# Kernel optimization log

Measured on AMD Instinct MI355X. Metric: run time of the kernel, lower is better.

## Reference

```python
import jax, jax.numpy as jnp
import numpy as np

B, D_IN, H, NZ, NC = 32768, 768, 2048, 128, 1024
EPS, NITERS = 0.5, 15


def setup_inputs() -> dict:
    key = jax.random.key(0)
    ks = jax.random.split(key, 4)
    x = jax.random.normal(ks[0], (B, D_IN), jnp.float32)
    # scaled init so feature magnitudes keep exp(-dist/eps) in f32 range
    W1 = jax.random.normal(ks[1], (D_IN, H), jnp.float32) / np.sqrt(D_IN)
    b1 = jnp.zeros((H,), jnp.float32)
    W2 = jax.random.normal(ks[2], (H, NZ), jnp.float32) / np.sqrt(H)
    b2 = jnp.zeros((NZ,), jnp.float32)
    centroids = jax.random.normal(ks[3], (NC, NZ), jnp.float32)
    return {
        'x': x, 'W1': W1, 'b1': b1, 'W2': W2, 'b2': b2,
        'centroids': centroids,
        'cluster_counts': jnp.zeros((NC,), jnp.int32),
        'raw_counts': jnp.zeros((NC,), jnp.int32),
        'total_soft_counts': jnp.zeros((NC,), jnp.float32),
    }


def _sinkhorn(scores, eps=EPS, niters=NITERS):
    # scores: [B, K].  Q: [K, B], matches torch reference where sum(Q) = col-sums.
    Q = jnp.exp(scores / eps).T
    Q = Q / jnp.sum(Q, axis=0, keepdims=True)
    K, Bb = Q.shape
    r = 1.0 / K
    c = 1.0 / Bb

    def body(Q, _):
        Q = Q * (r / jnp.sum(Q, axis=1))[:, None]
        Q = Q * (c / jnp.sum(Q, axis=0))[None, :]
        return Q, None

    Q, _ = jax.lax.scan(body, Q, None, length=niters)
    return (Q / jnp.sum(Q, axis=0, keepdims=True)).T  # [B, K]


def reference(x, W1, b1, W2, b2, centroids, cluster_counts, raw_counts, total_soft_counts):
    # fc backbone: Linear -> ReLU -> Linear
    fv = jax.nn.relu(x @ W1 + b1) @ W2 + b2                        # [B, nz]
    # pairwise euclidean distances to centroids (cdist via gram trick;
    # avoids materializing the [B, nc, nz] broadcast torch creates)
    sq = (jnp.sum(fv * fv, axis=1)[:, None]
          + jnp.sum(centroids * centroids, axis=1)[None, :]
          - 2.0 * fv @ centroids.T)
    cluster_dists = jnp.sqrt(jnp.maximum(sq, 1e-12))               # [B, nc]

    # sinkhorn branch (no_grad in torch)
    soft_assignments = jax.lax.stop_gradient(_sinkhorn(-cluster_dists))
    batch_assignments = jnp.argmin(soft_assignments, axis=1)       # [B]
    soft_counts = jnp.sum(soft_assignments, axis=0)                # [nc]
    # soft_train=False: gather assigned distances
    loss = jnp.mean(jnp.take_along_axis(cluster_dists, batch_assignments[:, None], axis=1))

    # scatter-accumulate counts
    new_raw = raw_counts.at[jnp.argmin(cluster_dists, axis=1)].add(1)
    new_cluster = cluster_counts.at[batch_assignments].add(1)
    new_total_soft = total_soft_counts + soft_counts
    return loss, batch_assignments, soft_counts, new_raw, new_cluster, new_total_soft
```

## Files before the change

### kernel.cpp

```cpp
#include <hip/hip_runtime.h>
#include <math.h>

#define BN    32768
#define DIN   768
#define HN    2048
#define NZ    128
#define NCN   1024

typedef __attribute__((ext_vector_type(8))) short s16x8;
typedef __attribute__((ext_vector_type(4))) float f32x4;
typedef unsigned short u16;

#define MFMA16(a,b,c) __builtin_amdgcn_mfma_f32_16x16x32_bf16(a,b,c,0,0,0)

__device__ __forceinline__ u16 bf16_rne(float x){
  unsigned u = __float_as_uint(x);
  unsigned r = (u + 0x7FFFu + ((u >> 16) & 1u)) >> 16;
  return (u16)r;
}
__device__ __forceinline__ float bf16_tof(u16 h){
  return __uint_as_float(((unsigned)h) << 16);
}
__device__ __forceinline__ void split3(float x, u16& h, u16& m, u16& l){
  h = bf16_rne(x);
  float r1 = x - bf16_tof(h);
  m = bf16_rne(r1);
  float r2 = r1 - bf16_tof(m);
  l = bf16_rne(r2);
}

__device__ __forceinline__ void gload16(const void* gsrc, void* lds){
  __builtin_amdgcn_global_load_lds(
      (const __attribute__((address_space(1))) unsigned int*)gsrc,
      (__attribute__((address_space(3))) unsigned int*)lds, 16, 0, 0);
}

__global__ __launch_bounds__(1024) void k0_init(float* u, int* hraw, int* hclu){
  const int k = threadIdx.x;
  u[k] = 1.0f;
  hraw[k] = 0;
  hclu[k] = 0;
}

__global__ __launch_bounds__(256) void c_split(
    const float* __restrict__ in, u16* __restrict__ oh, u16* __restrict__ om,
    u16* __restrict__ ol, int n4)
{
  const int i = blockIdx.x*256 + threadIdx.x;
  if (i >= n4) return;
  const f32x4 v = *(const f32x4*)&in[(size_t)i*4];
  ushort4 h4, m4, l4;
  split3(v[0], h4.x, m4.x, l4.x);
  split3(v[1], h4.y, m4.y, l4.y);
  split3(v[2], h4.z, m4.z, l4.z);
  split3(v[3], h4.w, m4.w, l4.w);
  *(ushort4*)&oh[(size_t)i*4] = h4;
  *(ushort4*)&om[(size_t)i*4] = m4;
  *(ushort4*)&ol[(size_t)i*4] = l4;
}

__global__ __launch_bounds__(256) void c_tsplit(
    const float* __restrict__ in, int R, int C,
    u16* __restrict__ oh, u16* __restrict__ om, u16* __restrict__ ol)
{
  __shared__ float L[64][65];
  const int t = threadIdx.x;
  const int bi = blockIdx.x, bj = blockIdx.y;
  #pragma unroll
  for (int m=0;m<4;++m){
    int flat = t + 256*m;
    int r = flat >> 4, c4 = (flat & 15) << 2;
    const float4 v = *(const float4*)&in[(size_t)(bi*64 + r)*C + bj*64 + c4];
    L[r][c4+0] = v.x; L[r][c4+1] = v.y; L[r][c4+2] = v.z; L[r][c4+3] = v.w;
  }
  __syncthreads();
  #pragma unroll
  for (int m=0;m<4;++m){
    int flat = t + 256*m;
    int oc = flat >> 4, k4 = (flat & 15) << 2;
    ushort4 h4, m4, l4;
    split3(L[k4+0][oc], h4.x, m4.x, l4.x);
    split3(L[k4+1][oc], h4.y, m4.y, l4.y);
    split3(L[k4+2][oc], h4.z, m4.z, l4.z);
    split3(L[k4+3][oc], h4.w, m4.w, l4.w);
    size_t off = (size_t)(bj*64 + oc)*R + bi*64 + k4;
    *(ushort4*)&oh[off] = h4;
    *(ushort4*)&om[off] = m4;
    *(ushort4*)&ol[off] = l4;
  }
}

__global__ __launch_bounds__(256) void c_norm(
    const float* __restrict__ in, float* __restrict__ out)
{
  const int w = threadIdx.x >> 6, l = threadIdx.x & 63;
  const int row = blockIdx.x*4 + w;
  const float2 v = *(const float2*)&in[(size_t)row*128 + l*2];
  float s = v.x*v.x + v.y*v.y;
  #pragma unroll
  for (int off=32; off; off>>=1) s += __shfl_xor(s, off, 64);
  if (l == 0) out[row] = s;
}

__global__ __launch_bounds__(256, 2) void k1_mfma(
    const u16* __restrict__ Xh, const u16* __restrict__ Xm, const u16* __restrict__ Xl,
    const u16* __restrict__ W1h, const u16* __restrict__ W1m, const u16* __restrict__ W1l,
    const float* __restrict__ b1,
    const u16* __restrict__ W2h, const u16* __restrict__ W2m, const u16* __restrict__ W2l,
    const float* __restrict__ b2, float* __restrict__ fv)
{
  __shared__ __align__(16) unsigned char sm[73728];
  unsigned char* xsr = sm;
  unsigned char* wsr = sm + 24576;

  const int t  = threadIdx.x;
  const int l  = t & 63;
  const int wn = t >> 6;
  const int g  = (l >> 4) & 3;
  const int lr = l & 15;
  const int row0 = blockIdx.x * 64;

  f32x4 fvacc[4][2];
  #pragma unroll
  for (int mf=0;mf<4;++mf){
    fvacc[mf][0] = (f32x4){0.f,0.f,0.f,0.f};
    fvacc[mf][1] = (f32x4){0.f,0.f,0.f,0.f};
  }

  #pragma unroll 1
  for (int nc = 0; nc < 16; ++nc){
    f32x4 a1acc[4][2];
    #pragma unroll
    for (int mf=0;mf<4;++mf){
      a1acc[mf][0] = (f32x4){0.f,0.f,0.f,0.f};
      a1acc[mf][1] = (f32x4){0.f,0.f,0.f,0.f};
    }

    #pragma unroll 1
    for (int ks = 0; ks < 12; ++ks){
      #pragma unroll
      for (int i=0;i<6;++i){
        const int ci = wn*6 + i;
        const int s  = ci >> 3;
        const int rb = ci & 7;
        const int xr = rb*8 + (l >> 3);
        const int q  = l & 7;
        const u16* Xp = (s==0) ? Xh : ((s==1) ? Xm : Xl);
        const u16* src = Xp + (size_t)(row0 + xr)*768 + ks*64 + ((q ^ (xr & 7)) << 3);
        gload16(src, xsr + s*8192 + rb*1024);
      }
      #pragma unroll
      for (int i=0;i<12;++i){
        const int ci = wn*12 + i;
        const int s  = ci >> 4;
        const int rb = ci & 15;
        const int rloc = rb*8 + (l >> 3);
        const int q  = l & 7;
        const u16* Wp = (s==0) ? W1h : ((s==1) ? W1m : W1l);
        const u16* src = Wp + (size_t)(nc*128 + rloc)*768 + ks*64 + ((q ^ (rloc & 7)) << 3);
        gload16(src, wsr + s*16384 + rb*1024);
      }
      __syncthreads();

      #pragma unroll
      for (int kk=0;kk<2;++kk){
        s16x8 Bf[3][2], Af[3][4];
        #pragma unroll
        for (int s=0;s<3;++s){
          #pragma unroll
          for (int nf=0;nf<2;++nf){
            const int br = wn*32 + nf*16 + lr;
            Bf[s][nf] = *(const s16x8*)(wsr + s*16384 + br*128 + ((16*(g + 4*kk)) ^ ((br & 7) << 4)));
          }
          #pragma unroll
          for (int mf=0;mf<4;++mf){
            const int ar = mf*16 + lr;
            Af[s][mf] = *(const s16x8*)(xsr + s*8192 + ar*128 + ((16*(g + 4*kk)) ^ ((ar & 7) << 4)));
          }
        }
        #pragma unroll
        for (int mf=0;mf<4;++mf){
          #pragma unroll
          for (int nf=0;nf<2;++nf){
            f32x4 acc = a1acc[mf][nf];
            acc = MFMA16(Af[0][mf], Bf[0][nf], acc);
            acc = MFMA16(Af[0][mf], Bf[1][nf], acc);
            acc = MFMA16(Af[1][mf], Bf[0][nf], acc);
            acc = MFMA16(Af[1][mf], Bf[1][nf], acc);
            acc = MFMA16(Af[0][mf], Bf[2][nf], acc);
            acc = MFMA16(Af[2][mf], Bf[0][nf], acc);
            a1acc[mf][nf] = acc;
          }
        }
      }
      __syncthreads();
    }

    const float b1v0 = b1[nc*128 + wn*32 + lr];
    const float b1v1 = b1[nc*128 + wn*32 + 16 + lr];

    #pragma unroll
    for (int half=0; half<2; ++half){
      if ((wn >> 1) == half){
        #pragma unroll
        for (int mf=0;mf<4;++mf){
          #pragma unroll
          for (int nf=0;nf<2;++nf){
            const int klocal = (wn & 1)*32 + nf*16 + lr;
            #pragma unroll
            for (int r=0;r<4;++r){
              float vv = a1acc[mf][nf][r] + ((nf==0) ? b1v0 : b1v1);
              vv = vv > 0.f ? vv : 0.f;
              u16 sh, sm2, sl;
              split3(vv, sh, sm2, sl);
              const int ar = mf*16 + g*4 + r;
              const int bo = ar*128 + ((2*klocal) ^ ((ar & 7) << 4));
              *(u16*)(xsr + bo)         = sh;
              *(u16*)(xsr + 8192 + bo)  = sm2;
              *(u16*)(xsr + 16384 + bo) = sl;
            }
          }
        }
      }
      #pragma unroll
      for (int i=0;i<12;++i){
        const int ci = wn*12 + i;
        const int s  = ci >> 4;
        const int rb = ci & 15;
        const int rloc = rb*8 + (l >> 3);
        const int q  = l & 7;
        const u16* Wp = (s==0) ? W2h : ((s==1) ? W2m : W2l);
        const u16* src = Wp + (size_t)rloc*2048 + nc*128 + half*64 + ((q ^ (rloc & 7)) << 3);
        gload16(src, wsr + s*16384 + rb*1024);
      }
      __syncthreads();

      #pragma unroll
      for (int kk=0;kk<2;++kk){
        s16x8 Bf[3][2], Af[3][4];
        #pragma unroll
        for (int s=0;s<3;++s){
          #pragma unroll
          for (int nf=0;nf<2;++nf){
            const int br = wn*32 + nf*16 + lr;
            Bf[s][nf] = *(const s16x8*)(wsr + s*16384 + br*128 + ((16*(g + 4*kk)) ^ ((br & 7) << 4)));
          }
          #pragma unroll
          for (int mf=0;mf<4;++mf){
            const int ar = mf*16 + lr;
            Af[s][mf] = *(const s16x8*)(xsr + s*8192 + ar*128 + ((16*(g + 4*kk)) ^ ((ar & 7) << 4)));
          }
        }
        #pragma unroll
        for (int mf=0;mf<4;++mf){
          #pragma unroll
          for (int nf=0;nf<2;++nf){
            f32x4 acc = fvacc[mf][nf];
            acc = MFMA16(Af[0][mf], Bf[0][nf], acc);
            acc = MFMA16(Af[0][mf], Bf[1][nf], acc);
            acc = MFMA16(Af[1][mf], Bf[0][nf], acc);
            acc = MFMA16(Af[1][mf], Bf[1][nf], acc);
            acc = MFMA16(Af[0][mf], Bf[2][nf], acc);
            acc = MFMA16(Af[2][mf], Bf[0][nf], acc);
            fvacc[mf][nf] = acc;
          }
        }
      }
      __syncthreads();
    }
  }

  const float b2v0 = b2[wn*32 + lr];
  const float b2v1 = b2[wn*32 + 16 + lr];
  #pragma unroll
  for (int mf=0;mf<4;++mf){
    #pragma unroll
    for (int nf=0;nf<2;++nf){
      #pragma unroll
      for (int r=0;r<4;++r){
        const int frow = row0 + mf*16 + g*4 + r;
        const int col  = wn*32 + nf*16 + lr;
        fv[(size_t)frow*NZ + col] = fvacc[mf][nf][r] + ((nf==0) ? b2v0 : b2v1);
      }
    }
  }
}

__global__ __launch_bounds__(256, 2) void k2_mfma(
    const u16* __restrict__ fvh, const u16* __restrict__ fvm, const u16* __restrict__ fvl,
    const u16* __restrict__ ch,  const u16* __restrict__ cm,  const u16* __restrict__ cl,
    const float* __restrict__ fvn, const float* __restrict__ cn,
    float* __restrict__ Q0)
{
  __shared__ __align__(16) unsigned char bs[49152];
  __shared__ float cnl[NCN];
  const int t  = threadIdx.x;
  const int l  = t & 63;
  const int wn = t >> 6;
  const int g  = (l >> 4) & 3;
  const int lr = l & 15;
  const int row0 = blockIdx.x * 64;
  const int arow = row0 + wn*16 + lr;

  s16x8 Af[3][4];
  #pragma unroll
  for (int kk=0;kk<4;++kk){
    const size_t ao = (size_t)arow*128 + kk*32 + g*8;
    Af[0][kk] = *(const s16x8*)&fvh[ao];
    Af[1][kk] = *(const s16x8*)&fvm[ao];
    Af[2][kk] = *(const s16x8*)&fvl[ao];
  }
  #pragma unroll
  for (int m=0;m<4;++m) cnl[t + 256*m] = cn[t + 256*m];
  const f32x4 fvnv = *(const f32x4*)&fvn[row0 + wn*16 + g*4];

  #pragma unroll 1
  for (int cc = 0; cc < NCN; cc += 64){
    #pragma unroll
    for (int i=0;i<12;++i){
      const int ci = wn*12 + i;
      const int s  = ci >> 4;
      const int rb = ci & 15;
      const int crow = rb*4 + (l >> 4);
      const int q  = l & 15;
      const u16* Cp = (s==0) ? ch : ((s==1) ? cm : cl);
      const u16* src = Cp + (size_t)(cc + crow)*128 + ((q ^ (crow & 15)) << 3);
      gload16(src, bs + s*16384 + rb*1024);
    }
    __syncthreads();

    f32x4 acc[4];
    #pragma unroll
    for (int nf=0;nf<4;++nf) acc[nf] = (f32x4){0.f,0.f,0.f,0.f};

    #pragma unroll
    for (int kk=0;kk<4;++kk){
      s16x8 Bq[3][4];
      #pragma unroll
      for (int nf=0;nf<4;++nf){
        const int br = nf*16 + lr;
        const int base = br*256 + (((g + 4*kk) ^ (br & 15)) << 4);
        Bq[0][nf] = *(const s16x8*)(bs + base);
        Bq[1][nf] = *(const s16x8*)(bs + 16384 + base);
        Bq[2][nf] = *(const s16x8*)(bs + 32768 + base);
      }
      #pragma unroll
      for (int nf=0;nf<4;++nf){
        f32x4 a = acc[nf];
        a = MFMA16(Af[0][kk], Bq[0][nf], a);
        a = MFMA16(Af[0][kk], Bq[1][nf], a);
        a = MFMA16(Af[1][kk], Bq[0][nf], a);
        a = MFMA16(Af[1][kk], Bq[1][nf], a);
        a = MFMA16(Af[0][kk], Bq[2][nf], a);
        a = MFMA16(Af[2][kk], Bq[0][nf], a);
        acc[nf] = a;
      }
    }

    #pragma unroll
    for (int nf=0;nf<4;++nf){
      const int n = cc + nf*16 + lr;
      const float cv = cnl[n];
      #pragma unroll
      for (int r=0;r<4;++r){
        float sq = fvnv[r] + cv - 2.0f*acc[nf][r];
        sq = sq > 1e-12f ? sq : 1e-12f;
        const float d = sqrtf(sq);
        Q0[(size_t)(row0 + wn*16 + g*4 + r)*NCN + n] = expf(-2.0f*d);
      }
    }
    __syncthreads();
  }
}

__global__ __launch_bounds__(256) void k3_pass(
    const float* __restrict__ Q0, const float* __restrict__ u,
    float* __restrict__ S_part, float alpha)
{
  __shared__ __align__(16) float ul[NCN];
  __shared__ __align__(16) float Sw[4][NCN];
  const int t = threadIdx.x;
  const int w = t >> 6, l = t & 63;
  #pragma unroll
  for (int m=0;m<4;++m) ul[t + 256*m] = u[t + 256*m];
  #pragma unroll
  for (int m=0;m<16;++m) (&Sw[0][0])[t + 256*m] = 0.f;
  __syncthreads();

  const float4* ul4 = (const float4*)ul;
  float4* Sw4 = (float4*)&Sw[w][0];
  const int gw = blockIdx.x*4 + w;
  const size_t b0 = (size_t)gw * 16;
  for (int rr=0; rr<16; ++rr){
    const float4* qrow = (const float4*)(Q0 + (b0 + rr)*NCN);
    float4 q4[4];
    float part = 0.f;
    #pragma unroll
    for (int j=0;j<4;++j){
      q4[j] = qrow[l + 64*j];
      float4 uu = ul4[l + 64*j];
      part += q4[j].x*uu.x; part += q4[j].y*uu.y;
      part += q4[j].z*uu.z; part += q4[j].w*uu.w;
    }
    #pragma unroll
    for (int off=32; off; off>>=1) part += __shfl_xor(part, off, 64);
    const float v = alpha / part;
    #pragma unroll
    for (int j=0;j<4;++j){
      float4 s = Sw4[l + 64*j];
      s.x += q4[j].x*v; s.y += q4[j].y*v; s.z += q4[j].z*v; s.w += q4[j].w*v;
      Sw4[l + 64*j] = s;
    }
  }
  __syncthreads();
  #pragma unroll
  for (int m=0;m<4;++m){
    int k = t + 256*m;
    S_part[(size_t)blockIdx.x*NCN + k] = ((Sw[0][k]+Sw[1][k])+(Sw[2][k]+Sw[3][k]));
  }
}

__global__ __launch_bounds__(256) void k4_unew(
    const float* __restrict__ S_part, float* __restrict__ u)
{
  __shared__ float P[4][64];
  const int t = threadIdx.x;
  const int col = blockIdx.x*64 + (t & 63);
  const int s4 = t >> 6;
  float p = 0.f;
  for (int i=0;i<128;++i)
    p += S_part[(size_t)(s4*128 + i)*NCN + col];
  P[s4][t & 63] = p;
  __syncthreads();
  if (s4 == 0){
    float tot = ((P[0][t] + P[1][t]) + (P[2][t] + P[3][t]));
    u[col] = (1.0f/1024.0f) / tot;
  }
}

__device__ __forceinline__ float comp4(const float4 v, int c){
  return (c==0)?v.x:(c==1)?v.y:(c==2)?v.z:v.w;
}

__global__ __launch_bounds__(256) void k5_final(
    const float* __restrict__ Q0, const float* __restrict__ u,
    float* __restrict__ softc_part, float* __restrict__ loss_part,
    int* __restrict__ hist_raw, int* __restrict__ hist_clu,
    float* __restrict__ out_ba)
{
  __shared__ __align__(16) float ul[NCN];
  __shared__ __align__(16) float Sw[4][NCN];
  __shared__ float lossw[4];
  const int t = threadIdx.x;
  const int w = t >> 6, l = t & 63;
  #pragma unroll
  for (int m=0;m<4;++m) ul[t + 256*m] = u[t + 256*m];
  #pragma unroll
  for (int m=0;m<16;++m) (&Sw[0][0])[t + 256*m] = 0.f;
  __syncthreads();

  const float4* ul4 = (const float4*)ul;
  float4* Sw4 = (float4*)&Sw[w][0];
  const int gw = blockIdx.x*4 + w;
  const size_t b0 = (size_t)gw * 32;
  float lacc = 0.f;
  for (int rr=0; rr<32; ++rr){
    const size_t b = b0 + rr;
    const float4* qrow = (const float4*)(Q0 + b*NCN);
    float4 q4[4], wv4[4];
    float part = 0.f;
    #pragma unroll
    for (int j=0;j<4;++j){
      q4[j] = qrow[l + 64*j];
      float4 uu = ul4[l + 64*j];
      wv4[j].x = uu.x*q4[j].x; wv4[j].y = uu.y*q4[j].y;
      wv4[j].z = uu.z*q4[j].z; wv4[j].w = uu.w*q4[j].w;
      part += wv4[j].x; part += wv4[j].y; part += wv4[j].z; part += wv4[j].w;
    }
    #pragma unroll
    for (int off=32; off; off>>=1) part += __shfl_xor(part, off, 64);
    const float inv = 1.0f / part;

    float smin = wv4[0].x * inv; int kmin = 4*l; float qat = q4[0].x;
    float qmax = q4[0].x;        int kmax = 4*l;
    #pragma unroll
    for (int j=0;j<4;++j){
      #pragma unroll
      for (int c=0;c<4;++c){
        if (j==0 && c==0) continue;
        float qv = comp4(q4[j], c);
        float sv = comp4(wv4[j], c) * inv;
        int k = 4*l + 256*j + c;
        if (sv < smin){ smin = sv; kmin = k; qat = qv; }
        if (qv > qmax){ qmax = qv; kmax = k; }
      }
    }
    #pragma unroll
    for (int off=32; off; off>>=1){
      float s2 = __shfl_xor(smin, off, 64);
      int   k2 = __shfl_xor(kmin, off, 64);
      float q2 = __shfl_xor(qat,  off, 64);
      if (s2 < smin || (s2 == smin && k2 < kmin)){ smin=s2; kmin=k2; qat=q2; }
      float m2 = __shfl_xor(qmax, off, 64);
      int   i2 = __shfl_xor(kmax, off, 64);
      if (m2 > qmax || (m2 == qmax && i2 < kmax)){ qmax=m2; kmax=i2; }
    }
    #pragma unroll
    for (int j=0;j<4;++j){
      float4 s = Sw4[l + 64*j];
      s.x += wv4[j].x*inv; s.y += wv4[j].y*inv;
      s.z += wv4[j].z*inv; s.w += wv4[j].w*inv;
      Sw4[l + 64*j] = s;
    }
    if (l == 0){
      out_ba[b] = (float)kmin;
      atomicAdd(&hist_clu[kmin], 1);
      atomicAdd(&hist_raw[kmax], 1);
      lacc += -0.5f * logf(qat);
    }
  }
  if (l == 0) lossw[w] = lacc;
  __syncthreads();
  #pragma unroll
  for (int m=0;m<4;++m){
    int k = t + 256*m;
    softc_part[(size_t)blockIdx.x*NCN + k] = ((Sw[0][k]+Sw[1][k])+(Sw[2][k]+Sw[3][k]));
  }
  if (t == 0) loss_part[blockIdx.x] = ((lossw[0]+lossw[1])+(lossw[2]+lossw[3]));
}

__global__ __launch_bounds__(1024) void k6_fin(
    const float* __restrict__ softc_part, const float* __restrict__ loss_part,
    const int* __restrict__ hist_raw, const int* __restrict__ hist_clu,
    const int* __restrict__ raw_in, const int* __restrict__ clu_in,
    const float* __restrict__ tsoft_in, float* __restrict__ out)
{
  const int k = threadIdx.x;
  float s0=0.f,s1=0.f,s2=0.f,s3=0.f;
  for (int blk=0; blk<256; blk+=4){
    s0 += softc_part[(size_t)(blk+0)*NCN + k];
    s1 += softc_part[(size_t)(blk+1)*NCN + k];
    s2 += softc_part[(size_t)(blk+2)*NCN + k];
    s3 += softc_part[(size_t)(blk+3)*NCN + k];
  }
  const float s = ((s0+s1)+(s2+s3));
  out[1 + BN + k]           = s;
  out[1 + BN + NCN + k]     = (float)(raw_in[k] + hist_raw[k]);
  out[1 + BN + 2*NCN + k]   = (float)(clu_in[k] + hist_clu[k]);
  out[1 + BN + 3*NCN + k]   = tsoft_in[k] + s;
  if (k == 0){
    float ls = 0.f;
    for (int i=0;i<256;++i) ls += loss_part[i];
    out[0] = ls / 32768.0f;
  }
}

extern "C" void kernel_launch(void* const* d_in, const int* in_sizes, int n_in,
                              void* d_out, int out_size, void* d_ws, size_t ws_size,
                              hipStream_t stream) {
  (void)in_sizes; (void)n_in; (void)out_size; (void)ws_size;
  const float* x      = (const float*)d_in[0];
  const float* W1     = (const float*)d_in[1];
  const float* b1     = (const float*)d_in[2];
  const float* W2     = (const float*)d_in[3];
  const float* b2     = (const float*)d_in[4];
  const float* cent   = (const float*)d_in[5];
  const int*   clu_in = (const int*)d_in[6];
  const int*   raw_in = (const int*)d_in[7];
  const float* tsoft  = (const float*)d_in[8];
  float* out = (float*)d_out;

  float* ws        = (float*)d_ws;
  float* fv        = ws;
  float* Q0        = ws + 4194304;
  u16*   Xh        = (u16*)Q0;
  u16*   Xm        = Xh + 25165824;
  u16*   Xl        = Xm + 25165824;
  float* u         = ws + 41943040;
  float* S_part    = u + 1024;
  float* softc_par = S_part + 524288;
  float* loss_par  = softc_par + 262144;
  int*   hist_raw  = (int*)(loss_par + 256);
  int*   hist_clu  = hist_raw + 1024;
  float* wbase     = (float*)(hist_clu + 1024);
  u16* W1Th = (u16*)wbase;
  u16* W1Tm = W1Th + 1572864;
  u16* W1Tl = W1Tm + 1572864;
  u16* W2Th = W1Tl + 1572864;
  u16* W2Tm = W2Th + 262144;
  u16* W2Tl = W2Tm + 262144;
  u16* fvh = (u16*)wbase;
  u16* fvm = fvh + 4194304;
  u16* fvl = fvm + 4194304;
  u16* ch  = fvl + 4194304;
  u16* cm  = ch  + 131072;
  u16* cl  = cm  + 131072;
  float* fvn = wbase + 6488064;
  float* cn  = fvn + 32768;

  c_split <<<24576, 256, 0, stream>>>(x, Xh, Xm, Xl, 6291456);
  c_tsplit<<<dim3(12, 32), 256, 0, stream>>>(W1, 768, 2048, W1Th, W1Tm, W1Tl);
  c_tsplit<<<dim3(32, 2),  256, 0, stream>>>(W2, 2048, 128, W2Th, W2Tm, W2Tl);
  k0_init<<<1, 1024, 0, stream>>>(u, hist_raw, hist_clu);

  k1_mfma<<<512, 256, 0, stream>>>(Xh, Xm, Xl, W1Th, W1Tm, W1Tl, b1,
                                   W2Th, W2Tm, W2Tl, b2, fv);

  c_split<<<4096, 256, 0, stream>>>(fv,   fvh, fvm, fvl, 1048576);
  c_split<<<128,  256, 0, stream>>>(cent, ch,  cm,  cl,  32768);
  c_norm <<<8192, 256, 0, stream>>>(fv,   fvn);
  c_norm <<<256,  256, 0, stream>>>(cent, cn);

  k2_mfma<<<512, 256, 0, stream>>>(fvh, fvm, fvl, ch, cm, cl, fvn, cn, Q0);

  for (int it = 0; it < 15; ++it){
    const float alpha = (it == 0) ? 1.0f : (1.0f/32768.0f);
    k3_pass<<<512, 256, 0, stream>>>(Q0, u, S_part, alpha);
    k4_unew<<<16, 256, 0, stream>>>(S_part, u);
  }
  k5_final<<<256, 256, 0, stream>>>(Q0, u, softc_par, loss_par,
                                    hist_raw, hist_clu, out + 1);
  k6_fin<<<1, 1024, 0, stream>>>(softc_par, loss_par, hist_raw, hist_clu,
                                 raw_in, clu_in, tsoft, out);
}
```

Before: 1.317 ms.

## Widen fc1 tile to 256 hidden cols and keep Sinkhorn accumulators in registers

The fused MLP kernel now computes 256 hidden columns per outer iteration instead of 128. Each loaded X k-slice is reused across two W1 sub-tiles, which halves the X reloads into shared memory, at the cost of twice as many accumulator registers. The Sinkhorn pass and final kernels keep u and the per-column sums in registers instead of shared memory, removing LDS read-modify-write traffic per row. The pass kernel also runs 256 blocks of 32 rows each, so k4 reduces only 256 partials.

```diff
diff --git a/kernel.cpp b/kernel.cpp
--- a/kernel.cpp
+++ b/kernel.cpp
@@ -128,13 +128,12 @@
   }
 
   #pragma unroll 1
-  for (int nc = 0; nc < 16; ++nc){
-    f32x4 a1acc[4][2];
-    #pragma unroll
-    for (int mf=0;mf<4;++mf){
-      a1acc[mf][0] = (f32x4){0.f,0.f,0.f,0.f};
-      a1acc[mf][1] = (f32x4){0.f,0.f,0.f,0.f};
-    }
+  for (int g0 = 0; g0 < 8; ++g0){
+    f32x4 a1acc[4][4];
+    #pragma unroll
+    for (int mf=0;mf<4;++mf)
+      #pragma unroll
+      for (int j=0;j<4;++j) a1acc[mf][j] = (f32x4){0.f,0.f,0.f,0.f};
 
     #pragma unroll 1
     for (int ks = 0; ks < 12; ++ks){
@@ -150,58 +149,77 @@
         gload16(src, xsr + s*8192 + rb*1024);
       }
       #pragma unroll
+      for (int sub2=0; sub2<2; ++sub2){
+        #pragma unroll
+        for (int i=0;i<12;++i){
+          const int ci = wn*12 + i;
+          const int s  = ci >> 4;
+          const int rb = ci & 15;
+          const int rloc = rb*8 + (l >> 3);
+          const int q  = l & 7;
+          const u16* Wp = (s==0) ? W1h : ((s==1) ? W1m : W1l);
+          const u16* src = Wp + (size_t)(g0*256 + sub2*128 + rloc)*768 + ks*64
+                              + ((q ^ (rloc & 7)) << 3);
+          gload16(src, wsr + s*16384 + rb*1024);
+        }
+        __syncthreads();
+
+        #pragma unroll
+        for (int kk=0;kk<2;++kk){
+          s16x8 Bf[3][2], Af[3][4];
+          #pragma unroll
+          for (int s=0;s<3;++s){
+            #pragma unroll
+            for (int nf=0;nf<2;++nf){
+              const int br = wn*32 + nf*16 + lr;
+              Bf[s][nf] = *(const s16x8*)(wsr + s*16384 + br*128 + ((16*(g + 4*kk)) ^ ((br & 7) << 4)));
+            }
+            #pragma unroll
+            for (int mf=0;mf<4;++mf){
+              const int ar = mf*16 + lr;
+              Af[s][mf] = *(const s16x8*)(xsr + s*8192 + ar*128 + ((16*(g + 4*kk)) ^ ((ar & 7) << 4)));
+            }
+          }
+          #pragma unroll
+          for (int mf=0;mf<4;++mf){
+            #pragma unroll
+            for (int nf=0;nf<2;++nf){
+              f32x4 acc = a1acc[mf][sub2*2+nf];
+              acc = MFMA16(Af[0][mf], Bf[0][nf], acc);
+              acc = MFMA16(Af[0][mf], Bf[1][nf], acc);
+              acc = MFMA16(Af[1][mf], Bf[0][nf], acc);
+              acc = MFMA16(Af[1][mf], Bf[1][nf], acc);
+              acc = MFMA16(Af[0][mf], Bf[2][nf], acc);
+              acc = MFMA16(Af[2][mf], Bf[0][nf], acc);
+              a1acc[mf][sub2*2+nf] = acc;
+            }
+          }
+        }
+        __syncthreads();
+      }
+    }
+
+    float b1v[2][2];
+    #pragma unroll
+    for (int s2=0;s2<2;++s2)
+      #pragma unroll
+      for (int nf=0;nf<2;++nf)
+        b1v[s2][nf] = b1[g0*256 + s2*128 + wn*32 + nf*16 + lr];
+
+    #pragma unroll
+    for (int h=0; h<4; ++h){
+      #pragma unroll
       for (int i=0;i<12;++i){
         const int ci = wn*12 + i;
         const int s  = ci >> 4;
         const int rb = ci & 15;
         const int rloc = rb*8 + (l >> 3);
         const int q  = l & 7;
-        const u16* Wp = (s==0) ? W1h : ((s==1) ? W1m : W1l);
-        const u16* src = Wp + (size_t)(nc*128 + rloc)*768 + ks*64 + ((q ^ (rloc & 7)) << 3);
+        const u16* Wp = (s==0) ? W2h : ((s==1) ? W2m : W2l);
+        const u16* src = Wp + (size_t)rloc*2048 + g0*256 + h*64 + ((q ^ (rloc & 7)) << 3);
         gload16(src, wsr + s*16384 + rb*1024);
       }
-      __syncthreads();
-
-      #pragma unroll
-      for (int kk=0;kk<2;++kk){
-        s16x8 Bf[3][2], Af[3][4];
-        #pragma unroll
-        for (int s=0;s<3;++s){
-          #pragma unroll
-          for (int nf=0;nf<2;++nf){
-            const int br = wn*32 + nf*16 + lr;
-            Bf[s][nf] = *(const s16x8*)(wsr + s*16384 + br*128 + ((16*(g + 4*kk)) ^ ((br & 7) << 4)));
-          }
-          #pragma unroll
-          for (int mf=0;mf<4;++mf){
-            const int ar = mf*16 + lr;
-            Af[s][mf] = *(const s16x8*)(xsr + s*8192 + ar*128 + ((16*(g + 4*kk)) ^ ((ar & 7) << 4)));
-          }
-        }
-        #pragma unroll
-        for (int mf=0;mf<4;++mf){
-          #pragma unroll
-          for (int nf=0;nf<2;++nf){
-            f32x4 acc = a1acc[mf][nf];
-            acc = MFMA16(Af[0][mf], Bf[0][nf], acc);
-            acc = MFMA16(Af[0][mf], Bf[1][nf], acc);
-            acc = MFMA16(Af[1][mf], Bf[0][nf], acc);
-            acc = MFMA16(Af[1][mf], Bf[1][nf], acc);
-            acc = MFMA16(Af[0][mf], Bf[2][nf], acc);
-            acc = MFMA16(Af[2][mf], Bf[0][nf], acc);
-            a1acc[mf][nf] = acc;
-          }
-        }
-      }
-      __syncthreads();
-    }
-
-    const float b1v0 = b1[nc*128 + wn*32 + lr];
-    const float b1v1 = b1[nc*128 + wn*32 + 16 + lr];
-
-    #pragma unroll
-    for (int half=0; half<2; ++half){
-      if ((wn >> 1) == half){
+      if ((wn >> 1) == (h & 1)){
         #pragma unroll
         for (int mf=0;mf<4;++mf){
           #pragma unroll
@@ -209,7 +227,7 @@
             const int klocal = (wn & 1)*32 + nf*16 + lr;
             #pragma unroll
             for (int r=0;r<4;++r){
-              float vv = a1acc[mf][nf][r] + ((nf==0) ? b1v0 : b1v1);
+              float vv = a1acc[mf][(h>>1)*2+nf][r] + b1v[h>>1][nf];
               vv = vv > 0.f ? vv : 0.f;
               u16 sh, sm2, sl;
               split3(vv, sh, sm2, sl);
@@ -221,17 +239,6 @@
             }
           }
         }
-      }
-      #pragma unroll
-      for (int i=0;i<12;++i){
-        const int ci = wn*12 + i;
-        const int s  = ci >> 4;
-        const int rb = ci & 15;
-        const int rloc = rb*8 + (l >> 3);
-        const int q  = l & 7;
-        const u16* Wp = (s==0) ? W2h : ((s==1) ? W2m : W2l);
-        const u16* src = Wp + (size_t)rloc*2048 + nc*128 + half*64 + ((q ^ (rloc & 7)) << 3);
-        gload16(src, wsr + s*16384 + rb*1024);
       }
       __syncthreads();
 
@@ -377,41 +384,40 @@
     const float* __restrict__ Q0, const float* __restrict__ u,
     float* __restrict__ S_part, float alpha)
 {
-  __shared__ __align__(16) float ul[NCN];
   __shared__ __align__(16) float Sw[4][NCN];
   const int t = threadIdx.x;
   const int w = t >> 6, l = t & 63;
-  #pragma unroll
-  for (int m=0;m<4;++m) ul[t + 256*m] = u[t + 256*m];
-  #pragma unroll
-  for (int m=0;m<16;++m) (&Sw[0][0])[t + 256*m] = 0.f;
-  __syncthreads();
-
-  const float4* ul4 = (const float4*)ul;
-  float4* Sw4 = (float4*)&Sw[w][0];
+
+  f32x4 uu[4], sacc[4];
+  #pragma unroll
+  for (int j=0;j<4;++j){
+    uu[j] = *(const f32x4*)&u[4*(l + 64*j)];
+    sacc[j] = (f32x4){0.f,0.f,0.f,0.f};
+  }
+
   const int gw = blockIdx.x*4 + w;
-  const size_t b0 = (size_t)gw * 16;
-  for (int rr=0; rr<16; ++rr){
-    const float4* qrow = (const float4*)(Q0 + (b0 + rr)*NCN);
-    float4 q4[4];
+  const size_t b0 = (size_t)gw * 32;
+  for (int rr=0; rr<32; ++rr){
+    const f32x4* qrow = (const f32x4*)(Q0 + (b0 + rr)*NCN);
+    f32x4 q4[4];
     float part = 0.f;
     #pragma unroll
     for (int j=0;j<4;++j){
       q4[j] = qrow[l + 64*j];
-      float4 uu = ul4[l + 64*j];
-      part += q4[j].x*uu.x; part += q4[j].y*uu.y;
-      part += q4[j].z*uu.z; part += q4[j].w*uu.w;
+      part += q4[j][0]*uu[j][0]; part += q4[j][1]*uu[j][1];
+      part += q4[j][2]*uu[j][2]; part += q4[j][3]*uu[j][3];
     }
     #pragma unroll
     for (int off=32; off; off>>=1) part += __shfl_xor(part, off, 64);
     const float v = alpha / part;
     #pragma unroll
     for (int j=0;j<4;++j){
-      float4 s = Sw4[l + 64*j];
-      s.x += q4[j].x*v; s.y += q4[j].y*v; s.z += q4[j].z*v; s.w += q4[j].w*v;
-      Sw4[l + 64*j] = s;
-    }
-  }
+      sacc[j][0] += q4[j][0]*v; sacc[j][1] += q4[j][1]*v;
+      sacc[j][2] += q4[j][2]*v; sacc[j][3] += q4[j][3]*v;
+    }
+  }
+  #pragma unroll
+  for (int j=0;j<4;++j) *(f32x4*)&Sw[w][4*(l + 64*j)] = sacc[j];
   __syncthreads();
   #pragma unroll
   for (int m=0;m<4;++m){
@@ -428,8 +434,8 @@
   const int col = blockIdx.x*64 + (t & 63);
   const int s4 = t >> 6;
   float p = 0.f;
-  for (int i=0;i<128;++i)
-    p += S_part[(size_t)(s4*128 + i)*NCN + col];
+  for (int i=0;i<64;++i)
+    p += S_part[(size_t)(s4*64 + i)*NCN + col];
   P[s4][t & 63] = p;
   __syncthreads();
   if (s4 == 0){
@@ -438,8 +444,8 @@
   }
 }
 
-__device__ __forceinline__ float comp4(const float4 v, int c){
-  return (c==0)?v.x:(c==1)?v.y:(c==2)?v.z:v.w;
+__device__ __forceinline__ float compv(const f32x4 v, int c){
+  return (c==0)?v[0]:(c==1)?v[1]:(c==2)?v[2]:v[3];
 }
 
 __global__ __launch_bounds__(256) void k5_final(
@@ -448,48 +454,46 @@
     int* __restrict__ hist_raw, int* __restrict__ hist_clu,
     float* __restrict__ out_ba)
 {
-  __shared__ __align__(16) float ul[NCN];
   __shared__ __align__(16) float Sw[4][NCN];
   __shared__ float lossw[4];
   const int t = threadIdx.x;
   const int w = t >> 6, l = t & 63;
-  #pragma unroll
-  for (int m=0;m<4;++m) ul[t + 256*m] = u[t + 256*m];
-  #pragma unroll
-  for (int m=0;m<16;++m) (&Sw[0][0])[t + 256*m] = 0.f;
-  __syncthreads();
-
-  const float4* ul4 = (const float4*)ul;
-  float4* Sw4 = (float4*)&Sw[w][0];
+
+  f32x4 uu[4], sacc[4];
+  #pragma unroll
+  for (int j=0;j<4;++j){
+    uu[j] = *(const f32x4*)&u[4*(l + 64*j)];
+    sacc[j] = (f32x4){0.f,0.f,0.f,0.f};
+  }
+
   const int gw = blockIdx.x*4 + w;
   const size_t b0 = (size_t)gw * 32;
   float lacc = 0.f;
   for (int rr=0; rr<32; ++rr){
     const size_t b = b0 + rr;
-    const float4* qrow = (const float4*)(Q0 + b*NCN);
-    float4 q4[4], wv4[4];
+    const f32x4* qrow = (const f32x4*)(Q0 + b*NCN);
+    f32x4 q4[4], wv4[4];
     float part = 0.f;
     #pragma unroll
     for (int j=0;j<4;++j){
       q4[j] = qrow[l + 64*j];
-      float4 uu = ul4[l + 64*j];
-      wv4[j].x = uu.x*q4[j].x; wv4[j].y = uu.y*q4[j].y;
-      wv4[j].z = uu.z*q4[j].z; wv4[j].w = uu.w*q4[j].w;
-      part += wv4[j].x; part += wv4[j].y; part += wv4[j].z; part += wv4[j].w;
+      wv4[j][0] = uu[j][0]*q4[j][0]; wv4[j][1] = uu[j][1]*q4[j][1];
+      wv4[j][2] = uu[j][2]*q4[j][2]; wv4[j][3] = uu[j][3]*q4[j][3];
+      part += wv4[j][0]; part += wv4[j][1]; part += wv4[j][2]; part += wv4[j][3];
     }
     #pragma unroll
     for (int off=32; off; off>>=1) part += __shfl_xor(part, off, 64);
     const float inv = 1.0f / part;
 
-    float smin = wv4[0].x * inv; int kmin = 4*l; float qat = q4[0].x;
-    float qmax = q4[0].x;        int kmax = 4*l;
+    float smin = wv4[0][0] * inv; int kmin = 4*l; float qat = q4[0][0];
+    float qmax = q4[0][0];        int kmax = 4*l;
     #pragma unroll
     for (int j=0;j<4;++j){
       #pragma unroll
       for (int c=0;c<4;++c){
         if (j==0 && c==0) continue;
-        float qv = comp4(q4[j], c);
-        float sv = comp4(wv4[j], c) * inv;
+        float qv = compv(q4[j], c);
+        float sv = compv(wv4[j], c) * inv;
         int k = 4*l + 256*j + c;
         if (sv < smin){ smin = sv; kmin = k; qat = qv; }
         if (qv > qmax){ qmax = qv; kmax = k; }
@@ -507,10 +511,8 @@
     }
     #pragma unroll
     for (int j=0;j<4;++j){
-      float4 s = Sw4[l + 64*j];
-      s.x += wv4[j].x*inv; s.y += wv4[j].y*inv;
-      s.z += wv4[j].z*inv; s.w += wv4[j].w*inv;
-      Sw4[l + 64*j] = s;
+      sacc[j][0] += wv4[j][0]*inv; sacc[j][1] += wv4[j][1]*inv;
+      sacc[j][2] += wv4[j][2]*inv; sacc[j][3] += wv4[j][3]*inv;
     }
     if (l == 0){
       out_ba[b] = (float)kmin;
@@ -519,6 +521,8 @@
       lacc += -0.5f * logf(qat);
     }
   }
+  #pragma unroll
+  for (int j=0;j<4;++j) *(f32x4*)&Sw[w][4*(l + 64*j)] = sacc[j];
   if (l == 0) lossw[w] = lacc;
   __syncthreads();
   #pragma unroll
@@ -615,7 +619,7 @@
 
   for (int it = 0; it < 15; ++it){
     const float alpha = (it == 0) ? 1.0f : (1.0f/32768.0f);
-    k3_pass<<<512, 256, 0, stream>>>(Q0, u, S_part, alpha);
+    k3_pass<<<256, 256, 0, stream>>>(Q0, u, S_part, alpha);
     k4_unew<<<16, 256, 0, stream>>>(S_part, u);
   }
   k5_final<<<256, 256, 0, stream>>>(Q0, u, softc_par, loss_par,
```

Result: slower. 1.454 ms (+10.4%).

## Fuse Sinkhorn iterations into one cooperative kernel keeping Q resident on-chip

Applied to the files above, without the earlier changes.

Replaces the 15 pairs of per-iteration pass and reduce kernels plus the final kernel with one cooperative kernel of 256 blocks. Each block holds its 128 rows of Q in registers and LDS across all iterations, so the 128MB Q matrix is read from HBM once instead of about 16 times. Column sums are exchanged through global memory with grid-wide syncs. The GEMM kernels also get a block-index swizzle that changes which rows each block handles. The risks are heavy register pressure (48 f32x4 per thread), 128KB+ of LDS, and the cost of about 30 grid syncs.

```diff
diff --git a/kernel.cpp b/kernel.cpp
--- a/kernel.cpp
+++ b/kernel.cpp
@@ -1,5 +1,8 @@
 #include <hip/hip_runtime.h>
+#include <hip/hip_cooperative_groups.h>
 #include <math.h>
+
+namespace cg = cooperative_groups;
 
 #define BN    32768
 #define DIN   768
@@ -33,6 +36,13 @@
   __builtin_amdgcn_global_load_lds(
       (const __attribute__((address_space(1))) unsigned int*)gsrc,
       (__attribute__((address_space(3))) unsigned int*)lds, 16, 0, 0);
+}
+
+__device__ __forceinline__ float agload(const float* p){
+  return __hip_atomic_load(p, __ATOMIC_RELAXED, __HIP_MEMORY_SCOPE_AGENT);
+}
+__device__ __forceinline__ void agstore(float* p, float v){
+  __hip_atomic_store(p, v, __ATOMIC_RELAXED, __HIP_MEMORY_SCOPE_AGENT);
 }
 
 __global__ __launch_bounds__(1024) void k0_init(float* u, int* hraw, int* hclu){
@@ -118,7 +128,9 @@
   const int wn = t >> 6;
   const int g  = (l >> 4) & 3;
   const int lr = l & 15;
-  const int row0 = blockIdx.x * 64;
+  const int bid = blockIdx.x;
+  const int swz = (bid & 7)*64 + (bid >> 3);
+  const int row0 = swz * 64;
 
   f32x4 fvacc[4][2];
   #pragma unroll
@@ -299,7 +311,9 @@
   const int wn = t >> 6;
   const int g  = (l >> 4) & 3;
   const int lr = l & 15;
-  const int row0 = blockIdx.x * 64;
+  const int bid = blockIdx.x;
+  const int swz = (bid & 7)*64 + (bid >> 3);
+  const int row0 = swz * 64;
   const int arow = row0 + wn*16 + lr;
 
   s16x8 Af[3][4];
@@ -373,124 +387,167 @@
   }
 }
 
-__global__ __launch_bounds__(256) void k3_pass(
-    const float* __restrict__ Q0, const float* __restrict__ u,
-    float* __restrict__ S_part, float alpha)
-{
-  __shared__ __align__(16) float ul[NCN];
-  __shared__ __align__(16) float Sw[4][NCN];
-  const int t = threadIdx.x;
-  const int w = t >> 6, l = t & 63;
-  #pragma unroll
-  for (int m=0;m<4;++m) ul[t + 256*m] = u[t + 256*m];
-  #pragma unroll
-  for (int m=0;m<16;++m) (&Sw[0][0])[t + 256*m] = 0.f;
-  __syncthreads();
-
-  const float4* ul4 = (const float4*)ul;
-  float4* Sw4 = (float4*)&Sw[w][0];
-  const int gw = blockIdx.x*4 + w;
-  const size_t b0 = (size_t)gw * 16;
-  for (int rr=0; rr<16; ++rr){
-    const float4* qrow = (const float4*)(Q0 + (b0 + rr)*NCN);
-    float4 q4[4];
-    float part = 0.f;
-    #pragma unroll
-    for (int j=0;j<4;++j){
-      q4[j] = qrow[l + 64*j];
-      float4 uu = ul4[l + 64*j];
-      part += q4[j].x*uu.x; part += q4[j].y*uu.y;
-      part += q4[j].z*uu.z; part += q4[j].w*uu.w;
-    }
-    #pragma unroll
-    for (int off=32; off; off>>=1) part += __shfl_xor(part, off, 64);
-    const float v = alpha / part;
-    #pragma unroll
-    for (int j=0;j<4;++j){
-      float4 s = Sw4[l + 64*j];
-      s.x += q4[j].x*v; s.y += q4[j].y*v; s.z += q4[j].z*v; s.w += q4[j].w*v;
-      Sw4[l + 64*j] = s;
-    }
-  }
-  __syncthreads();
-  #pragma unroll
-  for (int m=0;m<4;++m){
-    int k = t + 256*m;
-    S_part[(size_t)blockIdx.x*NCN + k] = ((Sw[0][k]+Sw[1][k])+(Sw[2][k]+Sw[3][k]));
-  }
-}
-
-__global__ __launch_bounds__(256) void k4_unew(
-    const float* __restrict__ S_part, float* __restrict__ u)
-{
-  __shared__ float P[4][64];
-  const int t = threadIdx.x;
-  const int col = blockIdx.x*64 + (t & 63);
-  const int s4 = t >> 6;
-  float p = 0.f;
-  for (int i=0;i<128;++i)
-    p += S_part[(size_t)(s4*128 + i)*NCN + col];
-  P[s4][t & 63] = p;
-  __syncthreads();
-  if (s4 == 0){
-    float tot = ((P[0][t] + P[1][t]) + (P[2][t] + P[3][t]));
-    u[col] = (1.0f/1024.0f) / tot;
-  }
-}
-
-__device__ __forceinline__ float comp4(const float4 v, int c){
-  return (c==0)?v.x:(c==1)?v.y:(c==2)?v.z:v.w;
-}
-
-__global__ __launch_bounds__(256) void k5_final(
-    const float* __restrict__ Q0, const float* __restrict__ u,
+__global__ __launch_bounds__(512, 1) void k35_coop(
+    const float* __restrict__ Q0, float* __restrict__ S_part,
+    float* __restrict__ ug,
     float* __restrict__ softc_part, float* __restrict__ loss_part,
     int* __restrict__ hist_raw, int* __restrict__ hist_clu,
     float* __restrict__ out_ba)
 {
-  __shared__ __align__(16) float ul[NCN];
-  __shared__ __align__(16) float Sw[4][NCN];
-  __shared__ float lossw[4];
+  __shared__ __align__(16) float Lq[32*1024];
+  __shared__ __align__(16) float Sbuf[1024];
+  __shared__ float lossw[8];
+  cg::grid_group grid = cg::this_grid();
+
   const int t = threadIdx.x;
   const int w = t >> 6, l = t & 63;
-  #pragma unroll
-  for (int m=0;m<4;++m) ul[t + 256*m] = u[t + 256*m];
-  #pragma unroll
-  for (int m=0;m<16;++m) (&Sw[0][0])[t + 256*m] = 0.f;
+  const int bid = blockIdx.x;
+  const int rowbase = bid*128 + w*16;
+
+  f32x4 qreg[48];
+  #pragma unroll
+  for (int r=0;r<12;++r){
+    const f32x4* qr = (const f32x4*)(Q0 + (size_t)(rowbase + r)*NCN);
+    #pragma unroll
+    for (int j=0;j<4;++j) qreg[r*4+j] = qr[l + 64*j];
+  }
+  f32x4* Lq4 = (f32x4*)Lq;
+  #pragma unroll
+  for (int r=0;r<4;++r){
+    const f32x4* qr = (const f32x4*)(Q0 + (size_t)(rowbase + 12 + r)*NCN);
+    #pragma unroll
+    for (int j=0;j<4;++j) Lq4[(w*4+r)*256 + l + 64*j] = qr[l + 64*j];
+  }
   __syncthreads();
 
-  const float4* ul4 = (const float4*)ul;
-  float4* Sw4 = (float4*)&Sw[w][0];
-  const int gw = blockIdx.x*4 + w;
-  const size_t b0 = (size_t)gw * 32;
+  f32x4 uu[4];
+  #pragma unroll
+  for (int j=0;j<4;++j) uu[j] = (f32x4){1.f,1.f,1.f,1.f};
+  f32x4* Sbuf4 = (f32x4*)Sbuf;
+
+  #pragma unroll 1
+  for (int it=0; it<15; ++it){
+    const float alpha = (it==0) ? 1.0f : (1.0f/32768.0f);
+    f32x4 sacc[4];
+    #pragma unroll
+    for (int j=0;j<4;++j) sacc[j] = (f32x4){0.f,0.f,0.f,0.f};
+
+    #pragma unroll
+    for (int r=0;r<12;++r){
+      float part = 0.f;
+      #pragma unroll
+      for (int j=0;j<4;++j){
+        part += qreg[r*4+j][0]*uu[j][0]; part += qreg[r*4+j][1]*uu[j][1];
+        part += qreg[r*4+j][2]*uu[j][2]; part += qreg[r*4+j][3]*uu[j][3];
+      }
+      #pragma unroll
+      for (int off=32; off; off>>=1) part += __shfl_xor(part, off, 64);
+      const float v = alpha / part;
+      #pragma unroll
+      for (int j=0;j<4;++j){
+        sacc[j][0] += qreg[r*4+j][0]*v; sacc[j][1] += qreg[r*4+j][1]*v;
+        sacc[j][2] += qreg[r*4+j][2]*v; sacc[j][3] += qreg[r*4+j][3]*v;
+      }
+    }
+    #pragma unroll
+    for (int r=0;r<4;++r){
+      f32x4 q4[4];
+      #pragma unroll
+      for (int j=0;j<4;++j) q4[j] = Lq4[(w*4+r)*256 + l + 64*j];
+      float part = 0.f;
+      #pragma unroll
+      for (int j=0;j<4;++j){
+        part += q4[j][0]*uu[j][0]; part += q4[j][1]*uu[j][1];
+        part += q4[j][2]*uu[j][2]; part += q4[j][3]*uu[j][3];
+      }
+      #pragma unroll
+      for (int off=32; off; off>>=1) part += __shfl_xor(part, off, 64);
+      const float v = alpha / part;
+      #pragma unroll
+      for (int j=0;j<4;++j){
+        sacc[j][0] += q4[j][0]*v; sacc[j][1] += q4[j][1]*v;
+        sacc[j][2] += q4[j][2]*v; sacc[j][3] += q4[j][3]*v;
+      }
+    }
+
+    #pragma unroll 1
+    for (int ww=0; ww<8; ++ww){
+      if (w == ww){
+        #pragma unroll
+        for (int j=0;j<4;++j){
+          if (ww == 0) Sbuf4[l + 64*j] = sacc[j];
+          else {
+            f32x4 s = Sbuf4[l + 64*j];
+            s[0]+=sacc[j][0]; s[1]+=sacc[j][1]; s[2]+=sacc[j][2]; s[3]+=sacc[j][3];
+            Sbuf4[l + 64*j] = s;
+          }
+        }
+      }
+      __syncthreads();
+    }
+    agstore(&S_part[(size_t)bid*NCN + t],       Sbuf[t]);
+    agstore(&S_part[(size_t)bid*NCN + t + 512], Sbuf[t + 512]);
+    __threadfence();
+    grid.sync();
+
+    if (t < 256){
+      #pragma unroll
+      for (int c=0;c<4;++c)
+        Sbuf[t*4+c] = agload(&S_part[(size_t)t*NCN + bid*4 + c]);
+    }
+    __syncthreads();
+    #pragma unroll 1
+    for (int s2=128; s2>0; s2>>=1){
+      if (t < s2*4){ const int i = t>>2, c = t&3; Sbuf[i*4+c] += Sbuf[(i+s2)*4+c]; }
+      __syncthreads();
+    }
+    if (t < 4) agstore(&ug[bid*4 + t], (1.0f/1024.0f)/Sbuf[t]);
+    __threadfence();
+    grid.sync();
+
+    Sbuf[t]       = agload(&ug[t]);
+    Sbuf[t + 512] = agload(&ug[t + 512]);
+    __syncthreads();
+    #pragma unroll
+    for (int j=0;j<4;++j) uu[j] = Sbuf4[l + 64*j];
+    __syncthreads();
+  }
+
+  f32x4 sacc[4];
+  #pragma unroll
+  for (int j=0;j<4;++j) sacc[j] = (f32x4){0.f,0.f,0.f,0.f};
   float lacc = 0.f;
-  for (int rr=0; rr<32; ++rr){
-    const size_t b = b0 + rr;
-    const float4* qrow = (const float4*)(Q0 + b*NCN);
-    float4 q4[4], wv4[4];
+
+  #pragma unroll
+  for (int r=0;r<16;++r){
+    f32x4 q4[4];
+    if (r < 12){
+      #pragma unroll
+      for (int j=0;j<4;++j) q4[j] = qreg[r*4+j];
+    } else {
+      #pragma unroll
+      for (int j=0;j<4;++j) q4[j] = Lq4[(w*4 + (r-12))*256 + l + 64*j];
+    }
     float part = 0.f;
     #pragma unroll
     for (int j=0;j<4;++j){
-      q4[j] = qrow[l + 64*j];
-      float4 uu = ul4[l + 64*j];
-      wv4[j].x = uu.x*q4[j].x; wv4[j].y = uu.y*q4[j].y;
-      wv4[j].z = uu.z*q4[j].z; wv4[j].w = uu.w*q4[j].w;
-      part += wv4[j].x; part += wv4[j].y; part += wv4[j].z; part += wv4[j].w;
+      part += uu[j][0]*q4[j][0]; part += uu[j][1]*q4[j][1];
+      part += uu[j][2]*q4[j][2]; part += uu[j][3]*q4[j][3];
     }
     #pragma unroll
     for (int off=32; off; off>>=1) part += __shfl_xor(part, off, 64);
     const float inv = 1.0f / part;
 
-    float smin = wv4[0].x * inv; int kmin = 4*l; float qat = q4[0].x;
-    float qmax = q4[0].x;        int kmax = 4*l;
+    float smin = (uu[0][0]*q4[0][0]) * inv; int kmin = 4*l; float qat = q4[0][0];
+    float qmax = q4[0][0];                  int kmax = 4*l;
     #pragma unroll
     for (int j=0;j<4;++j){
       #pragma unroll
       for (int c=0;c<4;++c){
         if (j==0 && c==0) continue;
-        float qv = comp4(q4[j], c);
-        float sv = comp4(wv4[j], c) * inv;
-        int k = 4*l + 256*j + c;
+        const float qv = q4[j][c];
+        const float sv = (uu[j][c]*qv) * inv;
+        const int k = 4*(l + 64*j) + c;
         if (sv < smin){ smin = sv; kmin = k; qat = qv; }
         if (qv > qmax){ qmax = qv; kmax = k; }
       }
@@ -507,26 +564,42 @@
     }
     #pragma unroll
     for (int j=0;j<4;++j){
-      float4 s = Sw4[l + 64*j];
-      s.x += wv4[j].x*inv; s.y += wv4[j].y*inv;
-      s.z += wv4[j].z*inv; s.w += wv4[j].w*inv;
-      Sw4[l + 64*j] = s;
+      sacc[j][0] += (uu[j][0]*q4[j][0])*inv; sacc[j][1] += (uu[j][1]*q4[j][1])*inv;
+      sacc[j][2] += (uu[j][2]*q4[j][2])*inv; sacc[j][3] += (uu[j][3]*q4[j][3])*inv;
     }
     if (l == 0){
-      out_ba[b] = (float)kmin;
+      const int row = rowbase + r;
+      out_ba[row] = (float)kmin;
       atomicAdd(&hist_clu[kmin], 1);
       atomicAdd(&hist_raw[kmax], 1);
       lacc += -0.5f * logf(qat);
     }
   }
+
   if (l == 0) lossw[w] = lacc;
-  __syncthreads();
-  #pragma unroll
-  for (int m=0;m<4;++m){
-    int k = t + 256*m;
-    softc_part[(size_t)blockIdx.x*NCN + k] = ((Sw[0][k]+Sw[1][k])+(Sw[2][k]+Sw[3][k]));
-  }
-  if (t == 0) loss_part[blockIdx.x] = ((lossw[0]+lossw[1])+(lossw[2]+lossw[3]));
+  #pragma unroll 1
+  for (int ww=0; ww<8; ++ww){
+    if (w == ww){
+      #pragma unroll
+      for (int j=0;j<4;++j){
+        if (ww == 0) Sbuf4[l + 64*j] = sacc[j];
+        else {
+          f32x4 s = Sbuf4[l + 64*j];
+          s[0]+=sacc[j][0]; s[1]+=sacc[j][1]; s[2]+=sacc[j][2]; s[3]+=sacc[j][3];
+          Sbuf4[l + 64*j] = s;
+        }
+      }
+    }
+    __syncthreads();
+  }
+  softc_part[(size_t)bid*NCN + t]       = Sbuf[t];
+  softc_part[(size_t)bid*NCN + t + 512] = Sbuf[t + 512];
+  if (t == 0){
+    float ls = 0.f;
+    #pragma unroll
+    for (int i=0;i<8;++i) ls += lossw[i];
+    loss_part[bid] = ls;
+  }
 }
 
 __global__ __launch_bounds__(1024) void k6_fin(
@@ -597,6 +670,7 @@
   u16* cl  = cm  + 131072;
   float* fvn = wbase + 6488064;
   float* cn  = fvn + 32768;
+  float* out_ba = out + 1;
 
   c_split <<<24576, 256, 0, stream>>>(x, Xh, Xm, Xl, 6291456);
   c_tsplit<<<dim3(12, 32), 256, 0, stream>>>(W1, 768, 2048, W1Th, W1Tm, W1Tl);
@@ -613,13 +687,15 @@
 
   k2_mfma<<<512, 256, 0, stream>>>(fvh, fvm, fvl, ch, cm, cl, fvn, cn, Q0);
 
-  for (int it = 0; it < 15; ++it){
-    const float alpha = (it == 0) ? 1.0f : (1.0f/32768.0f);
-    k3_pass<<<512, 256, 0, stream>>>(Q0, u, S_part, alpha);
-    k4_unew<<<16, 256, 0, stream>>>(S_part, u);
-  }
-  k5_final<<<256, 256, 0, stream>>>(Q0, u, softc_par, loss_par,
-                                    hist_raw, hist_clu, out + 1);
+  {
+    const float* Q0c = Q0;
+    void* kargs[] = { (void*)&Q0c, (void*)&S_part, (void*)&u,
+                      (void*)&softc_par, (void*)&loss_par,
+                      (void*)&hist_raw, (void*)&hist_clu, (void*)&out_ba };
+    hipLaunchCooperativeKernel((void*)k35_coop, dim3(256), dim3(512),
+                               kargs, 0, stream);
+  }
+
   k6_fin<<<1, 1024, 0, stream>>>(softc_par, loss_par, hist_raw, hist_clu,
                                  raw_in, clu_in, tsoft, out);
 }
```

Measured after the change: 3.161 ms. 140% more time.
